# Kernel optimization log

Measured on AMD Instinct MI355X. Metric: run time of the kernel, lower is better.

Reference implementation:

```python
import jax, jax.numpy as jnp
import numpy as np

# Static manifold selection per curvature (matches get_manifold): 0 -> Euclidean, <0 -> Lorentz(-k), >0 -> Sphere
CURVATURES = (0.0, -1.0, 1.0)
EPS = 1e-7

N_NODES = 8192
N_COMM = 16
D = 64


def _manifold_dist(k, x, c):
    """x: (N,d) nodes, c: (K,d) communities -> (N,K) distances."""
    if k == 0:
        diff = x[:, None, :] - c[None, :, :]          # (N,K,d)
        return jnp.linalg.norm(diff, axis=-1)
    elif k < 0:
        kk = -k                                       # Lorentz(-k), curvature -1/kk
        ip = x @ c.T                                  # Euclidean inner product (N,K)
        lip = ip - 2.0 * x[:, :1] * c[:, :1].T        # Lorentz inner: -x0*y0 + <rest>
        arg = jnp.maximum(-lip / kk, 1.0 + EPS)       # clamp for arcosh domain
        return jnp.sqrt(kk) * jnp.arccosh(arg)
    else:
        cos = jnp.clip(x @ c.T, -1.0 + EPS, 1.0 - EPS)
        return jnp.arccos(cos)


def setup_inputs() -> dict:
    key = jax.random.key(0)
    k1, k2, k3 = jax.random.split(key, 3)
    node_embeddings = jax.random.normal(k1, (len(CURVATURES), N_NODES, D), dtype=jnp.float32)
    community_embedding = jax.random.normal(k2, (N_COMM, D), dtype=jnp.float32)
    ricci = jax.random.normal(k3, (N_NODES, N_NODES), dtype=jnp.float32)
    alpha = jnp.array(1.0, dtype=jnp.float32)
    return {"node_embeddings": node_embeddings, "community_embedding": community_embedding,
            "ricci": ricci, "alpha": alpha}


def reference(node_embeddings, community_embedding, ricci, alpha):
    # per-manifold distances, stacked over curvatures -> (L, N, K)
    dists = jnp.stack([_manifold_dist(k, node_embeddings[i], community_embedding)
                       for i, k in enumerate(CURVATURES)], axis=0)
    dist_norm = jnp.sqrt(jnp.sum(dists * dists, axis=0))   # L2 norm over manifolds, (N, K)
    pi = jax.nn.softmax(dist_norm, axis=-1)                 # (N, K)
    N, K = pi.shape
    # intra_loss(pi).sum(-1).mean() == sum_{k,i,j} pi[i,k]*pi[j,k]*ricci[i,j] / (K*N)
    intra = jnp.einsum('ik,ij,jk->', pi, ricci, pi) / (K * N)
    # inter_loss(pi).sum(-1).mean() == sum_{k1,k2,i,j} pi[i,k1]*pi[j,k2]*ricci[i,j] / (K*K*N)
    s = pi.sum(axis=1)                                      # (N,)
    inter = (s @ (ricci @ s)) / (K * K * N)
    return alpha * intra - inter
```

## Files before the change

kernel.cpp:

```cpp
#include <hip/hip_runtime.h>
#include <math.h>

#define N_NODES 8192
#define N_COMM 16
#define DIMS 64
#define MROWS 4
#define JQ 4
#define JPI (256 * JQ)
#define ITERS (N_NODES / JPI)
#define PITS (N_NODES + 64)

typedef float v4f __attribute__((ext_vector_type(4)));

__global__ __launch_bounds__(256) void k_pi(
    const float* __restrict__ node,
    const float* __restrict__ comm,
    float* __restrict__ pi,
    float* __restrict__ piT)
{
  const int t = blockIdx.x * blockDim.x + threadIdx.x;
  const int i = t >> 4;
  const int k = t & 15;

  const float* xe = node + (size_t)i * DIMS;
  const float* xl = xe + (size_t)N_NODES * DIMS;
  const float* xs = xl + (size_t)N_NODES * DIMS;
  const float* c  = comm + k * DIMS;

  float de = 0.f, il = 0.f, isp = 0.f;
#pragma unroll
  for (int d = 0; d < DIMS; d += 4) {
    v4f a  = *(const v4f*)(xe + d);
    v4f b  = *(const v4f*)(xl + d);
    v4f e  = *(const v4f*)(xs + d);
    v4f cv = *(const v4f*)(c + d);
    v4f df = a - cv;
    de  += df.x * df.x + df.y * df.y + df.z * df.z + df.w * df.w;
    il  += b.x * cv.x + b.y * cv.y + b.z * cv.z + b.w * cv.w;
    isp += e.x * cv.x + e.y * cv.y + e.z * cv.z + e.w * cv.w;
  }

  float lip = il - 2.0f * xl[0] * c[0];
  float arg = fmaxf(-lip, 1.0f + 1e-7f);
  float d1  = acoshf(arg);
  float cs = fminf(fmaxf(isp, -1.0f + 1e-7f), 1.0f - 1e-7f);
  float d2 = acosf(cs);

  float dn = sqrtf(de + d1 * d1 + d2 * d2);

  float m = dn;
#pragma unroll
  for (int off = 1; off < 16; off <<= 1) m = fmaxf(m, __shfl_xor(m, off));
  float ex = expf(dn - m);
  float ss = ex;
#pragma unroll
  for (int off = 1; off < 16; off <<= 1) ss += __shfl_xor(ss, off);

  float v = ex / ss;
  pi[t] = v;
  piT[k * PITS + i] = v;
}

__global__ __launch_bounds__(256) void k_main(
    const float* __restrict__ ricci,
    const float* __restrict__ pi,
    const float* __restrict__ piT,
    double* __restrict__ accum)
{
  const int i0  = blockIdx.x * MROWS;
  const int tid = threadIdx.x;
  const int ph  = blockIdx.x & (ITERS - 1);
  const float* __restrict__ rbase = ricci + (size_t)i0 * N_NODES;

  float acc[MROWS][N_COMM] = {};
  v4f rv[2][MROWS];

  {
    const int j = ph * JPI + tid * JQ;
#pragma unroll
    for (int r = 0; r < MROWS; ++r)
      rv[0][r] = *(const v4f*)(rbase + (size_t)r * N_NODES + j);
  }

#pragma unroll
  for (int it = 0; it < ITERS; ++it) {
    const int cur = it & 1, nxt = cur ^ 1;
    const int j = ((it + ph) & (ITERS - 1)) * JPI + tid * JQ;

    v4f p[N_COMM];
#pragma unroll
    for (int k = 0; k < N_COMM; ++k)
      p[k] = *(const v4f*)(piT + (size_t)k * PITS + j);

    if (it + 1 < ITERS) {
      const int jn = ((it + 1 + ph) & (ITERS - 1)) * JPI + tid * JQ;
#pragma unroll
      for (int r = 0; r < MROWS; ++r)
        rv[nxt][r] = *(const v4f*)(rbase + (size_t)r * N_NODES + jn);
    }

#pragma unroll
    for (int k = 0; k < N_COMM; ++k) {
#pragma unroll
      for (int r = 0; r < MROWS; ++r) {
        v4f rr = rv[cur][r];
        acc[r][k] += rr.x * p[k].x + rr.y * p[k].y + rr.z * p[k].z + rr.w * p[k].w;
      }
    }
  }

  float fintra = 0.f, finter = 0.f;
#pragma unroll
  for (int r = 0; r < MROWS; ++r) {
#pragma unroll
    for (int k = 0; k < N_COMM; ++k) {
      fintra += pi[(i0 + r) * N_COMM + k] * acc[r][k];
      finter += acc[r][k];
    }
  }

  double di = (double)fintra, dn = (double)finter;
#pragma unroll
  for (int off = 32; off > 0; off >>= 1) {
    di += __shfl_down(di, off);
    dn += __shfl_down(dn, off);
  }
  __shared__ double red[8];
  const int w = tid >> 6;
  if ((tid & 63) == 0) { red[w] = di; red[4 + w] = dn; }
  __syncthreads();
  if (tid == 0) {
    atomicAdd(&accum[0], red[0] + red[1] + red[2] + red[3]);
    atomicAdd(&accum[1], red[4] + red[5] + red[6] + red[7]);
  }
}

__global__ void k_final(const double* __restrict__ accum,
                        const float* __restrict__ alpha,
                        float* __restrict__ out)
{
  const double KN  = (double)N_COMM * (double)N_NODES;
  const double KKN = (double)N_COMM * (double)N_COMM * (double)N_NODES;
  out[0] = (float)((double)alpha[0] * (accum[0] / KN) - accum[1] / KKN);
}

extern "C" void kernel_launch(void* const* d_in, const int* in_sizes, int n_in,
                              void* d_out, int out_size, void* d_ws, size_t ws_size,
                              hipStream_t stream) {
  (void)in_sizes; (void)n_in; (void)out_size; (void)ws_size;

  const float* node  = (const float*)d_in[0];
  const float* comm  = (const float*)d_in[1];
  const float* ricci = (const float*)d_in[2];
  const float* alpha = (const float*)d_in[3];
  float* out = (float*)d_out;

  double* accum = (double*)d_ws;
  float*  pi    = (float*)((char*)d_ws + 64);
  float*  piT   = (float*)((char*)d_ws + 64 + 524288);

  (void)hipMemsetAsync(d_ws, 0, 64, stream);

  hipLaunchKernelGGL(k_pi,   dim3((N_NODES * N_COMM) / 256), dim3(256), 0, stream,
                     node, comm, pi, piT);
  hipLaunchKernelGGL(k_main, dim3(N_NODES / MROWS), dim3(256), 0, stream,
                     ricci, pi, piT, accum);
  hipLaunchKernelGGL(k_final, dim3(1), dim3(1), 0, stream, accum, alpha, out);
}
```

Measured before the change: 400.0 us.

## Drop transposed pi copy, read row-major pi, fuse final reduction into main kernel

Removes the transposed piT buffer. The main kernel now reads the row-major pi directly, two j columns per thread, with v4f loads of 16 contiguous community values and vectorized accumulators. The memset and the final kernel are eliminated: zeroing moves into k_pi, and the last block, detected with an atomic counter, computes the output. This cuts two launches and the strided transposed writes, but halves the ricci vector width per thread and relies on the last-block-done pattern for correctness.

```diff
diff --git a/kernel.cpp b/kernel.cpp
--- a/kernel.cpp
+++ b/kernel.cpp
@@ -5,20 +5,22 @@
 #define N_COMM 16
 #define DIMS 64
 #define MROWS 4
-#define JQ 4
+#define JQ 2
 #define JPI (256 * JQ)
 #define ITERS (N_NODES / JPI)
-#define PITS (N_NODES + 64)
 
 typedef float v4f __attribute__((ext_vector_type(4)));
+typedef float v2f __attribute__((ext_vector_type(2)));
 
 __global__ __launch_bounds__(256) void k_pi(
     const float* __restrict__ node,
     const float* __restrict__ comm,
     float* __restrict__ pi,
-    float* __restrict__ piT)
+    double* __restrict__ accum,
+    unsigned* __restrict__ ctr)
 {
   const int t = blockIdx.x * blockDim.x + threadIdx.x;
+  if (t == 0) { accum[0] = 0.0; accum[1] = 0.0; *ctr = 0u; }
   const int i = t >> 4;
   const int k = t & 15;
 
@@ -56,30 +58,35 @@
 #pragma unroll
   for (int off = 1; off < 16; off <<= 1) ss += __shfl_xor(ss, off);
 
-  float v = ex / ss;
-  pi[t] = v;
-  piT[k * PITS + i] = v;
+  pi[t] = ex / ss;
 }
 
 __global__ __launch_bounds__(256) void k_main(
     const float* __restrict__ ricci,
     const float* __restrict__ pi,
-    const float* __restrict__ piT,
-    double* __restrict__ accum)
+    const float* __restrict__ alpha,
+    double* __restrict__ accum,
+    unsigned* __restrict__ ctr,
+    float* __restrict__ out)
 {
   const int i0  = blockIdx.x * MROWS;
   const int tid = threadIdx.x;
   const int ph  = blockIdx.x & (ITERS - 1);
   const float* __restrict__ rbase = ricci + (size_t)i0 * N_NODES;
 
-  float acc[MROWS][N_COMM] = {};
-  v4f rv[2][MROWS];
+  v4f acc[MROWS][4];
+#pragma unroll
+  for (int r = 0; r < MROWS; ++r)
+#pragma unroll
+    for (int q = 0; q < 4; ++q) acc[r][q] = (v4f)0.f;
+
+  v2f rv[2][MROWS];
 
   {
     const int j = ph * JPI + tid * JQ;
 #pragma unroll
     for (int r = 0; r < MROWS; ++r)
-      rv[0][r] = *(const v4f*)(rbase + (size_t)r * N_NODES + j);
+      rv[0][r] = *(const v2f*)(rbase + (size_t)r * N_NODES + j);
   }
 
 #pragma unroll
@@ -87,35 +94,40 @@
     const int cur = it & 1, nxt = cur ^ 1;
     const int j = ((it + ph) & (ITERS - 1)) * JPI + tid * JQ;
 
-    v4f p[N_COMM];
+    const float* pb = pi + (size_t)j * N_COMM;
+    v4f p0[4], p1[4];
 #pragma unroll
-    for (int k = 0; k < N_COMM; ++k)
-      p[k] = *(const v4f*)(piT + (size_t)k * PITS + j);
+    for (int q = 0; q < 4; ++q) p0[q] = *(const v4f*)(pb + 4 * q);
+#pragma unroll
+    for (int q = 0; q < 4; ++q) p1[q] = *(const v4f*)(pb + N_COMM + 4 * q);
 
     if (it + 1 < ITERS) {
       const int jn = ((it + 1 + ph) & (ITERS - 1)) * JPI + tid * JQ;
 #pragma unroll
       for (int r = 0; r < MROWS; ++r)
-        rv[nxt][r] = *(const v4f*)(rbase + (size_t)r * N_NODES + jn);
+        rv[nxt][r] = *(const v2f*)(rbase + (size_t)r * N_NODES + jn);
     }
 
 #pragma unroll
-    for (int k = 0; k < N_COMM; ++k) {
+    for (int r = 0; r < MROWS; ++r) {
+      const float rx = rv[cur][r].x;
+      const float ry = rv[cur][r].y;
 #pragma unroll
-      for (int r = 0; r < MROWS; ++r) {
-        v4f rr = rv[cur][r];
-        acc[r][k] += rr.x * p[k].x + rr.y * p[k].y + rr.z * p[k].z + rr.w * p[k].w;
-      }
+      for (int q = 0; q < 4; ++q)
+        acc[r][q] += rx * p0[q] + ry * p1[q];
     }
   }
 
   float fintra = 0.f, finter = 0.f;
 #pragma unroll
   for (int r = 0; r < MROWS; ++r) {
+    const float* pr = pi + (size_t)(i0 + r) * N_COMM;
 #pragma unroll
-    for (int k = 0; k < N_COMM; ++k) {
-      fintra += pi[(i0 + r) * N_COMM + k] * acc[r][k];
-      finter += acc[r][k];
+    for (int q = 0; q < 4; ++q) {
+      v4f pv = *(const v4f*)(pr + 4 * q);
+      v4f a  = acc[r][q];
+      fintra += pv.x * a.x + pv.y * a.y + pv.z * a.z + pv.w * a.w;
+      finter += a.x + a.y + a.z + a.w;
     }
   }
 
@@ -132,16 +144,17 @@
   if (tid == 0) {
     atomicAdd(&accum[0], red[0] + red[1] + red[2] + red[3]);
     atomicAdd(&accum[1], red[4] + red[5] + red[6] + red[7]);
+    __threadfence();
+    unsigned prev = atomicAdd(ctr, 1u);
+    if (prev == (unsigned)gridDim.x - 1u) {
+      __threadfence();
+      double ia = atomicAdd(&accum[0], 0.0);
+      double ir = atomicAdd(&accum[1], 0.0);
+      const double KN  = (double)N_COMM * (double)N_NODES;
+      const double KKN = (double)N_COMM * (double)N_COMM * (double)N_NODES;
+      out[0] = (float)((double)alpha[0] * (ia / KN) - ir / KKN);
+    }
   }
-}
-
-__global__ void k_final(const double* __restrict__ accum,
-                        const float* __restrict__ alpha,
-                        float* __restrict__ out)
-{
-  const double KN  = (double)N_COMM * (double)N_NODES;
-  const double KKN = (double)N_COMM * (double)N_COMM * (double)N_NODES;
-  out[0] = (float)((double)alpha[0] * (accum[0] / KN) - accum[1] / KKN);
 }
 
 extern "C" void kernel_launch(void* const* d_in, const int* in_sizes, int n_in,
@@ -155,15 +168,12 @@
   const float* alpha = (const float*)d_in[3];
   float* out = (float*)d_out;
 
-  double* accum = (double*)d_ws;
-  float*  pi    = (float*)((char*)d_ws + 64);
-  float*  piT   = (float*)((char*)d_ws + 64 + 524288);
-
-  (void)hipMemsetAsync(d_ws, 0, 64, stream);
+  double*   accum = (double*)d_ws;
+  unsigned* ctr   = (unsigned*)((char*)d_ws + 16);
+  float*    pi    = (float*)((char*)d_ws + 64);
 
   hipLaunchKernelGGL(k_pi,   dim3((N_NODES * N_COMM) / 256), dim3(256), 0, stream,
-                     node, comm, pi, piT);
+                     node, comm, pi, accum, ctr);
   hipLaunchKernelGGL(k_main, dim3(N_NODES / MROWS), dim3(256), 0, stream,
-                     ricci, pi, piT, accum);
-  hipLaunchKernelGGL(k_final, dim3(1), dim3(1), 0, stream, accum, alpha, out);
+                     ricci, pi, alpha, accum, ctr, out);
 }
```

After: 603.4 us. 1.51x slower.

## Retile ricci pass to hold piT columns in registers and fuse finalization

Applied to the files above, without the earlier changes.

The main kernel is retiled so each block owns a 1024-column slice and 32 rows. Its piT slice is loaded into registers once and reused across all rows, instead of reloading piT every iteration. The pi-weighted row reduction is applied on the fly, so the 64-float accumulator array disappears. The memset and the final kernel are removed: k_pi zeroes the accumulators, and the last block found by an atomic counter writes the output. This trades some pi row reloads and a global atomic counter for fewer launches and lower register pressure.

```diff
diff --git a/kernel.cpp b/kernel.cpp
--- a/kernel.cpp
+++ b/kernel.cpp
@@ -4,10 +4,10 @@
 #define N_NODES 8192
 #define N_COMM 16
 #define DIMS 64
-#define MROWS 4
-#define JQ 4
-#define JPI (256 * JQ)
-#define ITERS (N_NODES / JPI)
+#define ROWS 32
+#define JS 1024
+#define NJB (N_NODES / JS)
+#define NIB (N_NODES / ROWS)
 #define PITS (N_NODES + 64)
 
 typedef float v4f __attribute__((ext_vector_type(4)));
@@ -16,9 +16,12 @@
     const float* __restrict__ node,
     const float* __restrict__ comm,
     float* __restrict__ pi,
-    float* __restrict__ piT)
+    float* __restrict__ piT,
+    double* __restrict__ accum,
+    unsigned* __restrict__ ctr)
 {
   const int t = blockIdx.x * blockDim.x + threadIdx.x;
+  if (t == 0) { accum[0] = 0.0; accum[1] = 0.0; *ctr = 0u; }
   const int i = t >> 4;
   const int k = t & 15;
 
@@ -65,59 +68,57 @@
     const float* __restrict__ ricci,
     const float* __restrict__ pi,
     const float* __restrict__ piT,
-    double* __restrict__ accum)
+    const float* __restrict__ alpha,
+    double* __restrict__ accum,
+    unsigned* __restrict__ ctr,
+    float* __restrict__ out)
 {
-  const int i0  = blockIdx.x * MROWS;
   const int tid = threadIdx.x;
-  const int ph  = blockIdx.x & (ITERS - 1);
-  const float* __restrict__ rbase = ricci + (size_t)i0 * N_NODES;
+  const int jb  = blockIdx.x & (NJB - 1);
+  const int ib  = blockIdx.x >> 3;
+  const int i0  = ib * ROWS;
+  const int j   = jb * JS + tid * 4;
 
-  float acc[MROWS][N_COMM] = {};
-  v4f rv[2][MROWS];
+  v4f p[N_COMM];
+#pragma unroll
+  for (int k = 0; k < N_COMM; ++k)
+    p[k] = *(const v4f*)(piT + (size_t)k * PITS + j);
 
-  {
-    const int j = ph * JPI + tid * JQ;
-#pragma unroll
-    for (int r = 0; r < MROWS; ++r)
-      rv[0][r] = *(const v4f*)(rbase + (size_t)r * N_NODES + j);
-  }
+  const float* rptr = ricci + (size_t)i0 * N_NODES + j;
+
+  float fi[4] = {0.f, 0.f, 0.f, 0.f};
+  float finter = 0.f;
+
+  v4f rA = *(const v4f*)(rptr);
+  v4f rB = *(const v4f*)(rptr + N_NODES);
 
 #pragma unroll
-  for (int it = 0; it < ITERS; ++it) {
-    const int cur = it & 1, nxt = cur ^ 1;
-    const int j = ((it + ph) & (ITERS - 1)) * JPI + tid * JQ;
+  for (int ir = 0; ir < ROWS; ir += 2) {
+    const float* prow0 = pi + (size_t)(i0 + ir) * N_COMM;
+    const float* prow1 = prow0 + N_COMM;
 
-    v4f p[N_COMM];
-#pragma unroll
-    for (int k = 0; k < N_COMM; ++k)
-      p[k] = *(const v4f*)(piT + (size_t)k * PITS + j);
-
-    if (it + 1 < ITERS) {
-      const int jn = ((it + 1 + ph) & (ITERS - 1)) * JPI + tid * JQ;
-#pragma unroll
-      for (int r = 0; r < MROWS; ++r)
-        rv[nxt][r] = *(const v4f*)(rbase + (size_t)r * N_NODES + jn);
+    v4f r0 = rA, r1 = rB;
+    if (ir + 2 < ROWS) {
+      rA = *(const v4f*)(rptr + (size_t)(ir + 2) * N_NODES);
+      rB = *(const v4f*)(rptr + (size_t)(ir + 3) * N_NODES);
     }
 
 #pragma unroll
     for (int k = 0; k < N_COMM; ++k) {
+      float sk = r0.x * p[k].x + r0.y * p[k].y + r0.z * p[k].z + r0.w * p[k].w;
+      fi[k & 3] += prow0[k] * sk;
+    }
+    finter += (r0.x + r0.y) + (r0.z + r0.w);
+
 #pragma unroll
-      for (int r = 0; r < MROWS; ++r) {
-        v4f rr = rv[cur][r];
-        acc[r][k] += rr.x * p[k].x + rr.y * p[k].y + rr.z * p[k].z + rr.w * p[k].w;
-      }
+    for (int k = 0; k < N_COMM; ++k) {
+      float sk = r1.x * p[k].x + r1.y * p[k].y + r1.z * p[k].z + r1.w * p[k].w;
+      fi[k & 3] += prow1[k] * sk;
     }
+    finter += (r1.x + r1.y) + (r1.z + r1.w);
   }
 
-  float fintra = 0.f, finter = 0.f;
-#pragma unroll
-  for (int r = 0; r < MROWS; ++r) {
-#pragma unroll
-    for (int k = 0; k < N_COMM; ++k) {
-      fintra += pi[(i0 + r) * N_COMM + k] * acc[r][k];
-      finter += acc[r][k];
-    }
-  }
+  float fintra = (fi[0] + fi[1]) + (fi[2] + fi[3]);
 
   double di = (double)fintra, dn = (double)finter;
 #pragma unroll
@@ -132,16 +133,17 @@
   if (tid == 0) {
     atomicAdd(&accum[0], red[0] + red[1] + red[2] + red[3]);
     atomicAdd(&accum[1], red[4] + red[5] + red[6] + red[7]);
+    __threadfence();
+    unsigned prev = atomicAdd(ctr, 1u);
+    if (prev == (unsigned)gridDim.x - 1u) {
+      __threadfence();
+      double ia = atomicAdd(&accum[0], 0.0);
+      double ir = atomicAdd(&accum[1], 0.0);
+      const double KN  = (double)N_COMM * (double)N_NODES;
+      const double KKN = (double)N_COMM * (double)N_COMM * (double)N_NODES;
+      out[0] = (float)((double)alpha[0] * (ia / KN) - ir / KKN);
+    }
   }
-}
-
-__global__ void k_final(const double* __restrict__ accum,
-                        const float* __restrict__ alpha,
-                        float* __restrict__ out)
-{
-  const double KN  = (double)N_COMM * (double)N_NODES;
-  const double KKN = (double)N_COMM * (double)N_COMM * (double)N_NODES;
-  out[0] = (float)((double)alpha[0] * (accum[0] / KN) - accum[1] / KKN);
 }
 
 extern "C" void kernel_launch(void* const* d_in, const int* in_sizes, int n_in,
@@ -155,15 +157,13 @@
   const float* alpha = (const float*)d_in[3];
   float* out = (float*)d_out;
 
-  double* accum = (double*)d_ws;
-  float*  pi    = (float*)((char*)d_ws + 64);
-  float*  piT   = (float*)((char*)d_ws + 64 + 524288);
-
-  (void)hipMemsetAsync(d_ws, 0, 64, stream);
+  double*   accum = (double*)d_ws;
+  unsigned* ctr   = (unsigned*)((char*)d_ws + 16);
+  float*    pi    = (float*)((char*)d_ws + 64);
+  float*    piT   = (float*)((char*)d_ws + 64 + 524288);
 
   hipLaunchKernelGGL(k_pi,   dim3((N_NODES * N_COMM) / 256), dim3(256), 0, stream,
-                     node, comm, pi, piT);
-  hipLaunchKernelGGL(k_main, dim3(N_NODES / MROWS), dim3(256), 0, stream,
-                     ricci, pi, piT, accum);
-  hipLaunchKernelGGL(k_final, dim3(1), dim3(1), 0, stream, accum, alpha, out);
+                     node, comm, pi, piT, accum, ctr);
+  hipLaunchKernelGGL(k_main, dim3(NIB * NJB), dim3(256), 0, stream,
+                     ricci, pi, piT, alpha, accum, ctr, out);
 }
```

Measured after the change: 470.1 us. 1.18x slower.
